# Kernel optimization log

Measured on AMD Instinct MI355X. Metric: run time of the kernel, lower is better.

## Reference

```python
import jax, jax.numpy as jnp
import numpy as np


def _butter_bandpass_ba(N, w1, w2):
    """Digital Butterworth bandpass design (scipy.signal.iirfilter equivalent),
    fs = 2 half-cycles/sample, output='ba'. Done in float64 numpy at setup time."""
    # analog lowpass prototype (buttap): no zeros, N poles on unit circle, k=1
    p = -np.exp(1j * np.pi * np.arange(-N + 1, N, 2) / (2.0 * N))
    k = 1.0
    fs = 2.0
    warped = 2.0 * fs * np.tan(np.pi * np.array([w1, w2]) / fs)
    bw = warped[1] - warped[0]
    wo = np.sqrt(warped[0] * warped[1])
    # lp2bp_zpk
    p_lp = p * bw / 2.0
    sq = np.sqrt(p_lp ** 2 - wo ** 2)
    p_bp = np.concatenate([p_lp + sq, p_lp - sq])          # 2N poles
    z_bp = np.zeros(N, dtype=complex)                       # N zeros at origin
    k_bp = k * bw ** N
    # bilinear_zpk with fs=2
    fs2 = 2.0 * fs
    z_d = (fs2 + z_bp) / (fs2 - z_bp)
    p_d = (fs2 + p_bp) / (fs2 - p_bp)
    z_d = np.concatenate([z_d, -np.ones(len(p_bp) - len(z_bp))])
    k_d = k_bp * np.real(np.prod(fs2 - z_bp) / np.prod(fs2 - p_bp))
    b = np.real(k_d * np.poly(z_d))
    a = np.real(np.poly(p_d))
    return b, a


def setup_inputs() -> dict:
    key = jax.random.key(0)
    B, T = 512, 65536
    x = jax.random.normal(key, (B, T), dtype=jnp.float32)
    b_np, a_np = _butter_bandpass_ba(4, 0.1, 0.4)           # len 9 each
    return {
        "x": x,
        "b": jnp.asarray(b_np, dtype=jnp.float32),
        "a": jnp.asarray(a_np, dtype=jnp.float32),
    }


def _lfilter(x, b, a):
    """Direct-form II transposed IIR filter with zero initial state.
    x: (B, T); b, a: (M,). Equivalent to torchaudio lfilter (clamp=False)."""
    b = b / a[0]
    a = a / a[0]
    b0 = b[0]
    bt = b[1:]          # (M-1,)
    at = a[1:]          # (M-1,)

    def step(z, xt):
        # z: (B, M-1) delay state, xt: (B,)
        y = b0 * xt + z[:, 0]
        z_new = xt[:, None] * bt[None, :] - y[:, None] * at[None, :]
        z_new = z_new.at[:, :-1].add(z[:, 1:])
        return z_new, y

    z0 = jnp.zeros((x.shape[0], b.shape[0] - 1), dtype=x.dtype)
    _, y = jax.lax.scan(step, z0, x.T)                      # y: (T, B)
    return y.T


def reference(x, b, a):
    # filtfilt: forward pass, then filter the time-reversed result and reverse back
    y = _lfilter(x, b, a)
    y = _lfilter(y[:, ::-1], b, a)[:, ::-1]
    return y
```

## Files before the change

kernel.cpp:

```cpp
#include <hip/hip_runtime.h>

constexpr int CHUNK   = 32;
constexpr int WARM    = 96;
constexpr int BLOCK   = 64;
constexpr int NSTR    = 2;
constexpr int TILE    = BLOCK * NSTR * CHUNK;
constexpr int WARM_Q  = WARM / 4;
constexpr int TILE_Q  = TILE / 4;
constexpr int STAGE_Q = TILE_Q + WARM_Q;
constexpr int QPT     = CHUNK / 4;
constexpr int SITER   = (STAGE_Q + BLOCK - 1) / BLOCK;

typedef float v2 __attribute__((ext_vector_type(2)));

__device__ __forceinline__ int sw(int g) { return g ^ ((g >> 3) & 7); }

__device__ __forceinline__ v2 fma2(v2 a, v2 b, v2 c) {
#if defined(__has_builtin) && __has_builtin(__builtin_elementwise_fma)
    return __builtin_elementwise_fma(a, b, c);
#else
    return v2{fmaf(a.x, b.x, c.x), fmaf(a.y, b.y, c.y)};
#endif
}

template <int DIR>
__global__ __launch_bounds__(BLOCK, 2) void iir_pass(
    const float* __restrict__ x, float* __restrict__ y,
    const float* __restrict__ bc, const float* __restrict__ ac,
    int T, int tilesPerRow)
{
    __shared__ float4 lds[STAGE_Q];

    const int tid     = threadIdx.x;
    const int row     = blockIdx.x / tilesPerRow;
    const int tileIdx = blockIdx.x - row * tilesPerRow;
    const int tq0     = tileIdx * TILE_Q;

    const float* __restrict__ xr = x + (size_t)row * T;
    float* __restrict__       yr = y + (size_t)row * T;

    auto ldq = [&](int P) -> float4 {
        if (P < 0) return float4{0.f, 0.f, 0.f, 0.f};
        if (DIR == 0) return *(const float4*)(xr + 4 * P);
        return *(const float4*)(xr + (T - 4 - 4 * P));
    };

    float4 vr[SITER];
#pragma unroll
    for (int it = 0; it < SITER; ++it) {
        const int s = it * BLOCK + tid;
        if (s < STAGE_Q) vr[it] = ldq(tq0 + s - WARM_Q);
    }
#pragma unroll
    for (int it = 0; it < SITER; ++it) {
        const int s = it * BLOCK + tid;
        if (s < STAGE_Q) lds[sw(s)] = vr[it];
    }

    const float inv = 1.0f / ac[0];
    const v2 b02 = {bc[0] * inv, bc[0] * inv};
    v2 bt2[8], nat2[8];
#pragma unroll
    for (int i = 0; i < 8; ++i) {
        const float bi = bc[i + 1] * inv;
        const float ai = -(ac[i + 1] * inv);
        bt2[i]  = v2{bi, bi};
        nat2[i] = v2{ai, ai};
    }

    v2 z2[8];
#pragma unroll
    for (int i = 0; i < 8; ++i) z2[i] = v2{0.f, 0.f};

    auto step2 = [&](v2 xv) -> v2 {
        const v2 yv = fma2(b02, xv, z2[0]);
#pragma unroll
        for (int i = 0; i < 7; ++i)
            z2[i] = fma2(nat2[i], yv, fma2(bt2[i], xv, z2[i + 1]));
        z2[7] = fma2(nat2[7], yv, bt2[7] * xv);
        return yv;
    };

    __syncthreads();

    const int gA = QPT * tid;
    const int gB = QPT * tid + TILE_Q / 2;

#pragma unroll
    for (int i = 0; i < WARM_Q; ++i) {
        const float4 qA = lds[sw(gA + i)];
        const float4 qB = lds[sw(gB + i)];
        if (DIR == 0) {
            step2(v2{qA.x, qB.x}); step2(v2{qA.y, qB.y});
            step2(v2{qA.z, qB.z}); step2(v2{qA.w, qB.w});
        } else {
            step2(v2{qA.w, qB.w}); step2(v2{qA.z, qB.z});
            step2(v2{qA.y, qB.y}); step2(v2{qA.x, qB.x});
        }
    }

    __syncthreads();

#pragma unroll
    for (int j = 0; j < QPT; ++j) {
        const int ia = sw(gA + WARM_Q + j);
        const int ib = sw(gB + WARM_Q + j);
        const float4 qA = lds[ia];
        const float4 qB = lds[ib];
        v2 o0, o1, o2, o3;
        if (DIR == 0) {
            o0 = step2(v2{qA.x, qB.x}); o1 = step2(v2{qA.y, qB.y});
            o2 = step2(v2{qA.z, qB.z}); o3 = step2(v2{qA.w, qB.w});
        } else {
            o0 = step2(v2{qA.w, qB.w}); o1 = step2(v2{qA.z, qB.z});
            o2 = step2(v2{qA.y, qB.y}); o3 = step2(v2{qA.x, qB.x});
        }
        lds[ia] = float4{o0.x, o1.x, o2.x, o3.x};
        lds[ib] = float4{o0.y, o1.y, o2.y, o3.y};
    }

    __syncthreads();

#pragma unroll
    for (int k = 0; k < TILE_Q / BLOCK; ++k) {
        const int s = WARM_Q + k * BLOCK + tid;
        const float4 q = lds[sw(s)];
        const int P = tq0 + (s - WARM_Q);
        if (DIR == 0) *(float4*)(yr + 4 * P) = q;
        else *(float4*)(yr + (T - 4 - 4 * P)) = float4{q.w, q.z, q.y, q.x};
    }
}

extern "C" void kernel_launch(void* const* d_in, const int* in_sizes, int n_in,
                              void* d_out, int out_size, void* d_ws, size_t ws_size,
                              hipStream_t stream)
{
    const float* x = (const float*)d_in[0];
    const float* b = (const float*)d_in[1];
    const float* a = (const float*)d_in[2];
    float* out = (float*)d_out;
    float* tmp = (float*)d_ws;

    const int T = 65536;
    const int B = in_sizes[0] / T;
    const int tilesPerRow = T / TILE;
    const int totalBlocks = B * tilesPerRow;

    dim3 block(BLOCK);
    dim3 grid(totalBlocks);

    iir_pass<0><<<grid, block, 0, stream>>>(x,   tmp, b, a, T, tilesPerRow);
    iir_pass<1><<<grid, block, 0, stream>>>(tmp, out, b, a, T, tilesPerRow);
}
```

Baseline: 307.7 us.

## Fuse forward and backward IIR passes into one kernel with overlapped tiles

```diff
diff --git a/kernel.cpp b/kernel.cpp
--- a/kernel.cpp
+++ b/kernel.cpp
@@ -1,15 +1,19 @@
 #include <hip/hip_runtime.h>
 
-constexpr int CHUNK   = 32;
-constexpr int WARM    = 96;
-constexpr int BLOCK   = 64;
-constexpr int NSTR    = 2;
-constexpr int TILE    = BLOCK * NSTR * CHUNK;
-constexpr int WARM_Q  = WARM / 4;
-constexpr int TILE_Q  = TILE / 4;
-constexpr int STAGE_Q = TILE_Q + WARM_Q;
-constexpr int QPT     = CHUNK / 4;
-constexpr int SITER   = (STAGE_Q + BLOCK - 1) / BLOCK;
+constexpr int BLOCK    = 64;
+constexpr int NSTR     = 2;
+constexpr int NS       = BLOCK * NSTR;
+constexpr int CB       = 32;
+constexpr int CF       = 36;
+constexpr int TILE     = NS * CB;
+constexpr int WARM     = 96;
+constexpr int RF       = NS * CF;
+constexpr int IN_SAMP  = WARM + RF;
+constexpr int IN_Q     = IN_SAMP / 4;
+constexpr int WARM_Q   = WARM / 4;
+constexpr int QPT_F    = CF / 4;
+constexpr int QPT_B    = CB / 4;
+constexpr int SITER    = (IN_Q + BLOCK - 1) / BLOCK;
 
 typedef float v2 __attribute__((ext_vector_type(2)));
 
@@ -23,38 +27,35 @@
 #endif
 }
 
-template <int DIR>
-__global__ __launch_bounds__(BLOCK, 2) void iir_pass(
+__global__ __launch_bounds__(BLOCK, 2) void iir_fused(
     const float* __restrict__ x, float* __restrict__ y,
     const float* __restrict__ bc, const float* __restrict__ ac,
     int T, int tilesPerRow)
 {
-    __shared__ float4 lds[STAGE_Q];
+    __shared__ float4 lds[IN_Q];
 
     const int tid     = threadIdx.x;
     const int row     = blockIdx.x / tilesPerRow;
     const int tileIdx = blockIdx.x - row * tilesPerRow;
-    const int tq0     = tileIdx * TILE_Q;
+    const int t0      = tileIdx * TILE;
 
     const float* __restrict__ xr = x + (size_t)row * T;
     float* __restrict__       yr = y + (size_t)row * T;
 
-    auto ldq = [&](int P) -> float4 {
-        if (P < 0) return float4{0.f, 0.f, 0.f, 0.f};
-        if (DIR == 0) return *(const float4*)(xr + 4 * P);
-        return *(const float4*)(xr + (T - 4 - 4 * P));
-    };
-
     float4 vr[SITER];
 #pragma unroll
     for (int it = 0; it < SITER; ++it) {
-        const int s = it * BLOCK + tid;
-        if (s < STAGE_Q) vr[it] = ldq(tq0 + s - WARM_Q);
+        const int g = it * BLOCK + tid;
+        if (g < IN_Q) {
+            const int t = t0 - WARM + 4 * g;
+            vr[it] = (t < 0 || t >= T) ? float4{0.f, 0.f, 0.f, 0.f}
+                                       : *(const float4*)(xr + t);
+        }
     }
 #pragma unroll
     for (int it = 0; it < SITER; ++it) {
-        const int s = it * BLOCK + tid;
-        if (s < STAGE_Q) lds[sw(s)] = vr[it];
+        const int g = it * BLOCK + tid;
+        if (g < IN_Q) lds[sw(g)] = vr[it];
     }
 
     const float inv = 1.0f / ac[0];
@@ -69,9 +70,6 @@
     }
 
     v2 z2[8];
-#pragma unroll
-    for (int i = 0; i < 8; ++i) z2[i] = v2{0.f, 0.f};
-
     auto step2 = [&](v2 xv) -> v2 {
         const v2 yv = fma2(b02, xv, z2[0]);
 #pragma unroll
@@ -83,51 +81,81 @@
 
     __syncthreads();
 
-    const int gA = QPT * tid;
-    const int gB = QPT * tid + TILE_Q / 2;
+    const int sA = tid, sB = tid + BLOCK;
+
+#pragma unroll
+    for (int i = 0; i < 8; ++i) z2[i] = v2{0.f, 0.f};
 
 #pragma unroll
     for (int i = 0; i < WARM_Q; ++i) {
-        const float4 qA = lds[sw(gA + i)];
-        const float4 qB = lds[sw(gB + i)];
-        if (DIR == 0) {
-            step2(v2{qA.x, qB.x}); step2(v2{qA.y, qB.y});
-            step2(v2{qA.z, qB.z}); step2(v2{qA.w, qB.w});
-        } else {
-            step2(v2{qA.w, qB.w}); step2(v2{qA.z, qB.z});
-            step2(v2{qA.y, qB.y}); step2(v2{qA.x, qB.x});
-        }
+        const float4 qA = lds[sw(9 * sA + i)];
+        const float4 qB = lds[sw(9 * sB + i)];
+        step2(v2{qA.x, qB.x}); step2(v2{qA.y, qB.y});
+        step2(v2{qA.z, qB.z}); step2(v2{qA.w, qB.w});
+    }
+
+    __syncthreads();
+
+    const int vlim = T - t0;
+#pragma unroll
+    for (int j = 0; j < QPT_F; ++j) {
+        const int ia = sw(9 * sA + WARM_Q + j);
+        const int ib = sw(9 * sB + WARM_Q + j);
+        const float4 A = lds[ia];
+        const float4 B = lds[ib];
+        const v2 o0 = step2(v2{A.x, B.x});
+        const v2 o1 = step2(v2{A.y, B.y});
+        const v2 o2 = step2(v2{A.z, B.z});
+        const v2 o3 = step2(v2{A.w, B.w});
+        const int va = 36 * sA + 4 * j, vb = 36 * sB + 4 * j;
+        float4 ya, yb;
+        ya.x = (va + 0 < vlim) ? o0.x : 0.f;
+        ya.y = (va + 1 < vlim) ? o1.x : 0.f;
+        ya.z = (va + 2 < vlim) ? o2.x : 0.f;
+        ya.w = (va + 3 < vlim) ? o3.x : 0.f;
+        yb.x = (vb + 0 < vlim) ? o0.y : 0.f;
+        yb.y = (vb + 1 < vlim) ? o1.y : 0.f;
+        yb.z = (vb + 2 < vlim) ? o2.y : 0.f;
+        yb.w = (vb + 3 < vlim) ? o3.y : 0.f;
+        lds[ia] = ya;
+        lds[ib] = yb;
     }
 
     __syncthreads();
 
 #pragma unroll
-    for (int j = 0; j < QPT; ++j) {
-        const int ia = sw(gA + WARM_Q + j);
-        const int ib = sw(gB + WARM_Q + j);
-        const float4 qA = lds[ia];
-        const float4 qB = lds[ib];
-        v2 o0, o1, o2, o3;
-        if (DIR == 0) {
-            o0 = step2(v2{qA.x, qB.x}); o1 = step2(v2{qA.y, qB.y});
-            o2 = step2(v2{qA.z, qB.z}); o3 = step2(v2{qA.w, qB.w});
-        } else {
-            o0 = step2(v2{qA.w, qB.w}); o1 = step2(v2{qA.z, qB.z});
-            o2 = step2(v2{qA.y, qB.y}); o3 = step2(v2{qA.x, qB.x});
-        }
-        lds[ia] = float4{o0.x, o1.x, o2.x, o3.x};
-        lds[ib] = float4{o0.y, o1.y, o2.y, o3.y};
+    for (int i = 0; i < 8; ++i) z2[i] = v2{0.f, 0.f};
+
+#pragma unroll
+    for (int i = 0; i < WARM_Q; ++i) {
+        const float4 qA = lds[sw(24 + 8 * sA + 31 - i)];
+        const float4 qB = lds[sw(24 + 8 * sB + 31 - i)];
+        step2(v2{qA.w, qB.w}); step2(v2{qA.z, qB.z});
+        step2(v2{qA.y, qB.y}); step2(v2{qA.x, qB.x});
     }
 
     __syncthreads();
 
 #pragma unroll
-    for (int k = 0; k < TILE_Q / BLOCK; ++k) {
-        const int s = WARM_Q + k * BLOCK + tid;
-        const float4 q = lds[sw(s)];
-        const int P = tq0 + (s - WARM_Q);
-        if (DIR == 0) *(float4*)(yr + 4 * P) = q;
-        else *(float4*)(yr + (T - 4 - 4 * P)) = float4{q.w, q.z, q.y, q.x};
+    for (int j = 0; j < QPT_B; ++j) {
+        const int ia = sw(24 + 8 * sA + 7 - j);
+        const int ib = sw(24 + 8 * sB + 7 - j);
+        const float4 A = lds[ia];
+        const float4 B = lds[ib];
+        const v2 o0 = step2(v2{A.w, B.w});
+        const v2 o1 = step2(v2{A.z, B.z});
+        const v2 o2 = step2(v2{A.y, B.y});
+        const v2 o3 = step2(v2{A.x, B.x});
+        lds[ia] = float4{o3.x, o2.x, o1.x, o0.x};
+        lds[ib] = float4{o3.y, o2.y, o1.y, o0.y};
+    }
+
+    __syncthreads();
+
+#pragma unroll
+    for (int it = 0; it < TILE / 4 / BLOCK; ++it) {
+        const int q = it * BLOCK + tid;
+        *(float4*)(yr + t0 + 4 * q) = lds[sw(24 + q)];
     }
 }
 
@@ -139,7 +167,6 @@
     const float* b = (const float*)d_in[1];
     const float* a = (const float*)d_in[2];
     float* out = (float*)d_out;
-    float* tmp = (float*)d_ws;
 
     const int T = 65536;
     const int B = in_sizes[0] / T;
@@ -149,6 +176,5 @@
     dim3 block(BLOCK);
     dim3 grid(totalBlocks);
 
-    iir_pass<0><<<grid, block, 0, stream>>>(x,   tmp, b, a, T, tilesPerRow);
-    iir_pass<1><<<grid, block, 0, stream>>>(tmp, out, b, a, T, tilesPerRow);
+    iir_fused<<<grid, block, 0, stream>>>(x, out, b, a, T, tilesPerRow);
 }
```

New measurement: 285.0 us. 1.08x faster.
